# Optimization experiments

Measured on AMD Instinct MI355X. Metric: run time of the kernel, lower is better.

The kernel has to match this reference:

```python
import jax, jax.numpy as jnp
import numpy as np

B, I, H, L, D, O = 2048, 512, 512, 32, 1024, 512
TEMP = 1.0


def _make_params(key):
    ks = jax.random.split(key, 16)
    s = 0.05
    p = {}
    p['in_W'] = jax.random.normal(ks[0], (H, I), jnp.float32) * s
    p['in_b'] = jnp.zeros((H,), jnp.float32)
    p['out_W'] = jax.random.normal(ks[1], (O, H), jnp.float32) * s
    p['out_b'] = jnp.zeros((O,), jnp.float32)
    p['enc_Wih'] = jax.random.normal(ks[2], (4 * H, H), jnp.float32) * s
    p['enc_Whh'] = jax.random.normal(ks[3], (4 * H, H), jnp.float32) * s
    p['enc_bih'] = jnp.zeros((4 * H,), jnp.float32)
    p['enc_bhh'] = jnp.zeros((4 * H,), jnp.float32)
    p['dec_Wih'] = jax.random.normal(ks[4], (4 * H, H), jnp.float32) * s
    p['dec_Whh'] = jax.random.normal(ks[5], (4 * H, H), jnp.float32) * s
    p['dec_bih'] = jnp.zeros((4 * H,), jnp.float32)
    p['dec_bhh'] = jnp.zeros((4 * H,), jnp.float32)
    p['h2t_W'] = jax.random.normal(ks[6], (D, H), jnp.float32) * s
    p['h2t_b'] = jnp.zeros((D,), jnp.float32)
    p['t2h_W'] = jax.random.normal(ks[7], (H, D), jnp.float32) * s
    p['t2h_b'] = jnp.zeros((H,), jnp.float32)
    return p


def setup_inputs() -> dict:
    key = jax.random.key(0)
    k1, k2, k3 = jax.random.split(key, 3)
    inp = {'x': jax.random.normal(k1, (B, I), jnp.float32),
           'gumbel': jax.random.gumbel(k2, (L, B, D), jnp.float32)}
    inp.update(_make_params(k3))
    return inp


def _lstm_cell(x, h, c, Wih, Whh, bih, bhh):
    gates = x @ Wih.T + bih + h @ Whh.T + bhh  # [B, 4H]
    i, f, g, o = jnp.split(gates, 4, axis=-1)
    i = jax.nn.sigmoid(i); f = jax.nn.sigmoid(f)
    g = jnp.tanh(g); o = jax.nn.sigmoid(o)
    c_new = f * c + i * g
    h_new = o * jnp.tanh(c_new)
    return h_new, c_new


def reference(x, gumbel, in_W, in_b, out_W, out_b,
              enc_Wih, enc_Whh, enc_bih, enc_bhh,
              dec_Wih, dec_Whh, dec_bih, dec_bhh,
              h2t_W, h2t_b, t2h_W, t2h_b):
    # ---- encode ----
    x_emb = x @ in_W.T + in_b                      # [B, H]
    hx0 = jnp.zeros((B, H), x.dtype)
    inp0 = jnp.zeros((B, H), x.dtype)

    def enc_step(carry, g_noise):
        hx, cx, inp = carry
        hx, cx = _lstm_cell(inp, hx, cx, enc_Wih, enc_Whh, enc_bih, enc_bhh)
        pre = hx @ h2t_W.T + h2t_b                 # [B, D]
        soft = jax.nn.softmax((pre + g_noise) / TEMP, axis=-1)
        amax = jnp.argmax(soft, axis=-1)           # [B]
        oh = jax.nn.one_hot(amax, D, dtype=soft.dtype)
        z = soft + jax.lax.stop_gradient(oh - soft)  # straight-through
        inp = z @ t2h_W.T + t2h_b
        return (hx, cx, inp), (z, pre, amax)

    # initial cell state is the embedded input (cx = x), per the source
    _, (z_seq, logit_seq, msg_seq) = jax.lax.scan(
        enc_step, (hx0, x_emb, inp0), gumbel)
    one_hot = jnp.transpose(z_seq, (1, 0, 2))      # [B, L, D]
    logits = jnp.transpose(logit_seq, (1, 0, 2))   # [B, L, D]
    messages = msg_seq.T                           # [B, L]

    # ---- decode ----
    z_emb = z_seq @ t2h_W.T + t2h_b                # [L, B, H]

    def dec_step(carry, inp):
        hx, cx = carry
        hx, cx = _lstm_cell(inp, hx, cx, dec_Wih, dec_Whh, dec_bih, dec_bhh)
        return (hx, cx), None

    (hx_final, _), _ = jax.lax.scan(
        dec_step, (jnp.zeros((B, H), x.dtype), jnp.zeros((B, H), x.dtype)), z_emb)
    recon = hx_final @ out_W.T + out_b             # [B, O]
    return recon, one_hot, logits, messages
```

## Files before the change

kernel.cpp:

```cpp
#include <hip/hip_runtime.h>
#include <math.h>

#define B_  2048
#define I_  512
#define H_  512
#define L_  32
#define D_  1024
#define O_  512
#define H4_ 2048
#define KC  32

typedef _Float16 f16x8 __attribute__((ext_vector_type(8)));
typedef _Float16 f16x4 __attribute__((ext_vector_type(4)));
typedef float    f32x4 __attribute__((ext_vector_type(4)));

#define SPLIT_S  1024.0f
#define SPLIT_RS 0.0009765625f

__global__ __launch_bounds__(256) void gemm_atb(
    const float* __restrict__ A, const float* __restrict__ W,
    const float* __restrict__ bias, float* __restrict__ C, int ldc,
    float* __restrict__ C2, int ldc2,
    int M, int N, int K)
{
    __shared__ __align__(16) float As[KC][68];
    __shared__ __align__(16) float Ws[KC][68];
    const int tx = threadIdx.x & 15, ty = threadIdx.x >> 4;
    const int m0 = blockIdx.y * 64, n0 = blockIdx.x * 64;
    float acc[4][4] = {};

    for (int k0 = 0; k0 < K; k0 += KC) {
#pragma unroll
        for (int p = 0; p < 2; ++p) {
            int q = threadIdx.x + 256 * p;
            int r = q >> 3, c = q & 7;
            float4 va = *reinterpret_cast<const float4*>(
                &A[(long long)(m0 + r) * K + k0 + c * 4]);
            As[c * 4 + 0][r] = va.x; As[c * 4 + 1][r] = va.y;
            As[c * 4 + 2][r] = va.z; As[c * 4 + 3][r] = va.w;
            float4 vw = *reinterpret_cast<const float4*>(
                &W[(long long)(n0 + r) * K + k0 + c * 4]);
            Ws[c * 4 + 0][r] = vw.x; Ws[c * 4 + 1][r] = vw.y;
            Ws[c * 4 + 2][r] = vw.z; Ws[c * 4 + 3][r] = vw.w;
        }
        __syncthreads();
#pragma unroll
        for (int kk = 0; kk < KC; ++kk) {
            float4 a = *reinterpret_cast<const float4*>(&As[kk][ty * 4]);
            float4 w = *reinterpret_cast<const float4*>(&Ws[kk][tx * 4]);
            float av[4] = {a.x, a.y, a.z, a.w};
            float wv[4] = {w.x, w.y, w.z, w.w};
#pragma unroll
            for (int i = 0; i < 4; ++i)
#pragma unroll
                for (int j = 0; j < 4; ++j)
                    acc[i][j] = fmaf(av[i], wv[j], acc[i][j]);
        }
        __syncthreads();
    }

#pragma unroll
    for (int i = 0; i < 4; ++i) {
        int m = m0 + ty * 4 + i;
        int n = n0 + tx * 4;
        float4 out;
        out.x = acc[i][0]; out.y = acc[i][1]; out.z = acc[i][2]; out.w = acc[i][3];
        if (bias) {
            out.x += bias[n + 0]; out.y += bias[n + 1];
            out.z += bias[n + 2]; out.w += bias[n + 3];
        }
        *reinterpret_cast<float4*>(&C[(long long)m * ldc + n]) = out;
        if (C2)
            *reinterpret_cast<float4*>(&C2[(long long)m * ldc2 + n]) = out;
    }
}

__global__ __launch_bounds__(256) void split_f16(
    const float* __restrict__ src, _Float16* __restrict__ d1,
    _Float16* __restrict__ d2, int n4)
{
    int i = blockIdx.x * 256 + threadIdx.x;
    if (i >= n4) return;
    float4 v = reinterpret_cast<const float4*>(src)[i];
    float vv[4] = {v.x, v.y, v.z, v.w};
    f16x4 o1, o2;
#pragma unroll
    for (int j = 0; j < 4; ++j) {
        _Float16 hh = (_Float16)vv[j];
        o1[j] = hh;
        o2[j] = (_Float16)((vv[j] - (float)hh) * SPLIT_S);
    }
    *reinterpret_cast<f16x4*>(d1 + 4 * i) = o1;
    *reinterpret_cast<f16x4*>(d2 + 4 * i) = o2;
}

__global__ __launch_bounds__(512) void lstm_step_mfma(
    const _Float16* __restrict__ hx1, const _Float16* __restrict__ hx2,
    float* __restrict__ cx,
    const _Float16* __restrict__ W1, const _Float16* __restrict__ W2,
    const float* __restrict__ P,
    const int* __restrict__ m_prev,
    const float* __restrict__ bih, const float* __restrict__ bhh,
    _Float16* __restrict__ ho1, _Float16* __restrict__ ho2,
    float* __restrict__ hof)
{
    __shared__ __align__(16) _Float16 As1[128][72];
    __shared__ __align__(16) _Float16 As2[128][72];
    __shared__ __align__(16) _Float16 Ws1[128][72];
    __shared__ __align__(16) _Float16 Ws2[128][72];
    __shared__ int ms[128];

    const int tid = threadIdx.x;
    const int m0 = blockIdx.y * 128, h0 = blockIdx.x * 32;
    const int l = tid & 63, wid = tid >> 6;
    const int wm = wid >> 1, wn = wid & 1;

    if (m_prev != nullptr && tid < 128) ms[tid] = m_prev[m0 + tid];

    f32x4 accM[2][4] = {};
    f32x4 accC[2][4] = {};

    for (int k0 = 0; k0 < H_; k0 += 64) {
#pragma unroll
        for (int cc = 0; cc < 2; ++cc) {
            int c = tid + cc * 512;
            int r = c >> 3, q = (c & 7) << 3;
            size_t ga = (size_t)(m0 + r) * H_ + k0 + q;
            *(uint4*)&As1[r][q] = *(const uint4*)(hx1 + ga);
            *(uint4*)&As2[r][q] = *(const uint4*)(hx2 + ga);
            int wrow = ((r >> 4) & 3) * H_ + h0 + ((r >> 6) << 4) + (r & 15);
            size_t gw = (size_t)wrow * H_ + k0 + q;
            *(uint4*)&Ws1[r][q] = *(const uint4*)(W1 + gw);
            *(uint4*)&Ws2[r][q] = *(const uint4*)(W2 + gw);
        }
        __syncthreads();
        const int ac = (l >> 4) << 3;
        const int arow = wm * 32 + (l & 15);
        const int brow = wn * 64 + (l & 15);
#pragma unroll
        for (int kc = 0; kc < 2; ++kc) {
            int ko = kc * 32 + ac;
            f16x8 b1[4], b2[4];
#pragma unroll
            for (int fn = 0; fn < 4; ++fn) {
                b1[fn] = *(const f16x8*)&Ws1[brow + fn * 16][ko];
                b2[fn] = *(const f16x8*)&Ws2[brow + fn * 16][ko];
            }
#pragma unroll
            for (int fm = 0; fm < 2; ++fm) {
                f16x8 a1 = *(const f16x8*)&As1[arow + fm * 16][ko];
                f16x8 a2 = *(const f16x8*)&As2[arow + fm * 16][ko];
#pragma unroll
                for (int fn = 0; fn < 4; ++fn) {
                    accM[fm][fn] = __builtin_amdgcn_mfma_f32_16x16x32_f16(
                        a1, b1[fn], accM[fm][fn], 0, 0, 0);
                    accC[fm][fn] = __builtin_amdgcn_mfma_f32_16x16x32_f16(
                        a1, b2[fn], accC[fm][fn], 0, 0, 0);
                    accC[fm][fn] = __builtin_amdgcn_mfma_f32_16x16x32_f16(
                        a2, b1[fn], accC[fm][fn], 0, 0, 0);
                }
            }
        }
        __syncthreads();
    }

    const int hl = l & 15;
    const int h  = h0 + wn * 16 + hl;
    const int rb = m0 + wm * 32 + ((l >> 4) << 2);
    float bs0 = bih[0 * H_ + h] + bhh[0 * H_ + h];
    float bs1 = bih[1 * H_ + h] + bhh[1 * H_ + h];
    float bs2 = bih[2 * H_ + h] + bhh[2 * H_ + h];
    float bs3 = bih[3 * H_ + h] + bhh[3 * H_ + h];
#pragma unroll
    for (int fm = 0; fm < 2; ++fm) {
#pragma unroll
        for (int rg = 0; rg < 4; ++rg) {
            int b = rb + fm * 16 + rg;
            float g0 = accM[fm][0][rg] + SPLIT_RS * accC[fm][0][rg] + bs0;
            float g1 = accM[fm][1][rg] + SPLIT_RS * accC[fm][1][rg] + bs1;
            float g2 = accM[fm][2][rg] + SPLIT_RS * accC[fm][2][rg] + bs2;
            float g3 = accM[fm][3][rg] + SPLIT_RS * accC[fm][3][rg] + bs3;
            if (m_prev != nullptr) {
                const float* Pr = P + (size_t)ms[b - m0] * H4_;
                g0 += Pr[0 * H_ + h]; g1 += Pr[1 * H_ + h];
                g2 += Pr[2 * H_ + h]; g3 += Pr[3 * H_ + h];
            }
            float ig = 1.f / (1.f + expf(-g0));
            float fg = 1.f / (1.f + expf(-g1));
            float gg = tanhf(g2);
            float og = 1.f / (1.f + expf(-g3));
            size_t off = (size_t)b * H_ + h;
            float cnew = fg * cx[off] + ig * gg;
            cx[off] = cnew;
            float hv = og * tanhf(cnew);
            _Float16 hh1 = (_Float16)hv;
            ho1[off] = hh1;
            ho2[off] = (_Float16)((hv - (float)hh1) * SPLIT_S);
            if (hof != nullptr) hof[off] = hv;
        }
    }
}

__global__ __launch_bounds__(256) void gemm_pre_mfma(
    const _Float16* __restrict__ A1, const _Float16* __restrict__ A2,
    const _Float16* __restrict__ W1, const _Float16* __restrict__ W2,
    const float* __restrict__ bias,
    float* __restrict__ C,
    float* __restrict__ C2, int ldc2)
{
    __shared__ __align__(16) _Float16 As1[64][72];
    __shared__ __align__(16) _Float16 As2[64][72];
    __shared__ __align__(16) _Float16 Ws1[128][72];
    __shared__ __align__(16) _Float16 Ws2[128][72];

    const int tid = threadIdx.x;
    const int m0 = blockIdx.y * 64, n0 = blockIdx.x * 128;
    const int l = tid & 63, wid = tid >> 6;
    const int wm = wid >> 1, wn = wid & 1;

    f32x4 accM[2][4] = {};
    f32x4 accC[2][4] = {};

    for (int k0 = 0; k0 < H_; k0 += 64) {
#pragma unroll
        for (int cc = 0; cc < 2; ++cc) {
            int c = tid + cc * 256;
            int r = c >> 3, q = (c & 7) << 3;
            size_t ga = (size_t)(m0 + r) * H_ + k0 + q;
            *(uint4*)&As1[r][q] = *(const uint4*)(A1 + ga);
            *(uint4*)&As2[r][q] = *(const uint4*)(A2 + ga);
        }
#pragma unroll
        for (int cc = 0; cc < 4; ++cc) {
            int c = tid + cc * 256;
            int r = c >> 3, q = (c & 7) << 3;
            size_t gw = (size_t)(n0 + r) * H_ + k0 + q;
            *(uint4*)&Ws1[r][q] = *(const uint4*)(W1 + gw);
            *(uint4*)&Ws2[r][q] = *(const uint4*)(W2 + gw);
        }
        __syncthreads();
        const int ac = (l >> 4) << 3;
        const int arow = wm * 32 + (l & 15);
        const int brow = wn * 64 + (l & 15);
#pragma unroll
        for (int kc = 0; kc < 2; ++kc) {
            int ko = kc * 32 + ac;
            f16x8 b1[4], b2[4];
#pragma unroll
            for (int fn = 0; fn < 4; ++fn) {
                b1[fn] = *(const f16x8*)&Ws1[brow + fn * 16][ko];
                b2[fn] = *(const f16x8*)&Ws2[brow + fn * 16][ko];
            }
#pragma unroll
            for (int fm = 0; fm < 2; ++fm) {
                f16x8 a1 = *(const f16x8*)&As1[arow + fm * 16][ko];
                f16x8 a2 = *(const f16x8*)&As2[arow + fm * 16][ko];
#pragma unroll
                for (int fn = 0; fn < 4; ++fn) {
                    accM[fm][fn] = __builtin_amdgcn_mfma_f32_16x16x32_f16(
                        a1, b1[fn], accM[fm][fn], 0, 0, 0);
                    accC[fm][fn] = __builtin_amdgcn_mfma_f32_16x16x32_f16(
                        a1, b2[fn], accC[fm][fn], 0, 0, 0);
                    accC[fm][fn] = __builtin_amdgcn_mfma_f32_16x16x32_f16(
                        a2, b1[fn], accC[fm][fn], 0, 0, 0);
                }
            }
        }
        __syncthreads();
    }

    const int hl = l & 15;
    const int rb = m0 + wm * 32 + ((l >> 4) << 2);
#pragma unroll
    for (int fn = 0; fn < 4; ++fn) {
        int d = n0 + wn * 64 + fn * 16 + hl;
        float bv = bias[d];
#pragma unroll
        for (int fm = 0; fm < 2; ++fm)
#pragma unroll
            for (int rg = 0; rg < 4; ++rg) {
                int b = rb + fm * 16 + rg;
                float v = accM[fm][fn][rg] + SPLIT_RS * accC[fm][fn][rg] + bv;
                C[(size_t)b * D_ + d] = v;
                C2[(size_t)b * ldc2 + d] = v;
            }
    }
}

__global__ __launch_bounds__(256) void argmax_step(
    const float* __restrict__ pre, const float* __restrict__ gum,
    float* __restrict__ onehot, float* __restrict__ messages,
    int* __restrict__ m_out, int l)
{
    const int wave = threadIdx.x >> 6, lane = threadIdx.x & 63;
    const int b = blockIdx.x * 4 + wave;
    const float* pr = pre + (long long)b * D_;
    const float* gr = gum + (long long)b * D_;
    float best = -INFINITY; int bi = 0;
#pragma unroll
    for (int j = 0; j < D_ / 64; ++j) {
        int idx = lane + j * 64;
        float v = pr[idx] + gr[idx];
        if (v > best) { best = v; bi = idx; }
    }
#pragma unroll
    for (int off = 32; off > 0; off >>= 1) {
        float ov = __shfl_down(best, off);
        int   oi = __shfl_down(bi, off);
        if (ov > best || (ov == best && oi < bi)) { best = ov; bi = oi; }
    }
    if (lane == 0) {
        m_out[b] = bi;
        messages[(long long)b * L_ + l] = (float)bi;
        onehot[((long long)b * L_ + l) * D_ + bi] = 1.0f;
    }
}

__global__ __launch_bounds__(256) void build_emb(
    const float* __restrict__ t2h_W, const float* __restrict__ t2h_b,
    float* __restrict__ emb)
{
    int idx = blockIdx.x * 256 + threadIdx.x;
    int d = idx >> 9, h = idx & (H_ - 1);
    emb[idx] = t2h_W[(long long)h * D_ + d] + t2h_b[h];
}

extern "C" void kernel_launch(void* const* d_in, const int* in_sizes, int n_in,
                              void* d_out, int out_size, void* d_ws, size_t ws_size,
                              hipStream_t stream)
{
    (void)in_sizes; (void)n_in; (void)out_size; (void)ws_size;
    const float* x       = (const float*)d_in[0];
    const float* gumbel  = (const float*)d_in[1];
    const float* in_W    = (const float*)d_in[2];
    const float* in_b    = (const float*)d_in[3];
    const float* out_W   = (const float*)d_in[4];
    const float* out_b   = (const float*)d_in[5];
    const float* enc_Wih = (const float*)d_in[6];
    const float* enc_Whh = (const float*)d_in[7];
    const float* enc_bih = (const float*)d_in[8];
    const float* enc_bhh = (const float*)d_in[9];
    const float* dec_Wih = (const float*)d_in[10];
    const float* dec_Whh = (const float*)d_in[11];
    const float* dec_bih = (const float*)d_in[12];
    const float* dec_bhh = (const float*)d_in[13];
    const float* h2t_W   = (const float*)d_in[14];
    const float* h2t_b   = (const float*)d_in[15];
    const float* t2h_W   = (const float*)d_in[16];
    const float* t2h_b   = (const float*)d_in[17];

    float* out      = (float*)d_out;
    float* recon    = out;
    float* onehot   = out + (size_t)B_ * O_;
    float* logits   = onehot + (size_t)B_ * L_ * D_;
    float* messages = logits + (size_t)B_ * L_ * D_;

    float* ws    = (float*)d_ws;
    float* cx    = ws;
    float* pre   = cx + (size_t)B_ * H_;
    float* emb   = pre + (size_t)B_ * D_;
    float* P_enc = emb + (size_t)D_ * H_;
    float* P_dec = P_enc + (size_t)D_ * H4_;
    float* hxf   = P_dec + (size_t)D_ * H4_;
    int*   m_all = (int*)(hxf + (size_t)B_ * H_);
    _Float16* fb   = (_Float16*)(m_all + (size_t)L_ * B_);
    _Float16* hxA1 = fb;  fb += (size_t)B_ * H_;
    _Float16* hxA2 = fb;  fb += (size_t)B_ * H_;
    _Float16* hxB1 = fb;  fb += (size_t)B_ * H_;
    _Float16* hxB2 = fb;  fb += (size_t)B_ * H_;
    _Float16* encW1 = fb; fb += (size_t)H4_ * H_;
    _Float16* encW2 = fb; fb += (size_t)H4_ * H_;
    _Float16* decW1 = fb; fb += (size_t)H4_ * H_;
    _Float16* decW2 = fb; fb += (size_t)H4_ * H_;
    _Float16* h2t1  = fb; fb += (size_t)D_ * H_;
    _Float16* h2t2  = fb;

    const dim3 blk256(256);

    hipMemsetAsync(hxA1, 0, (size_t)B_ * H_ * 4, stream);
    hipMemsetAsync(onehot, 0, (size_t)B_ * L_ * D_ * sizeof(float), stream);

    split_f16<<<dim3((H4_ * H_ / 4) / 256), blk256, 0, stream>>>(
        enc_Whh, encW1, encW2, H4_ * H_ / 4);
    split_f16<<<dim3((H4_ * H_ / 4) / 256), blk256, 0, stream>>>(
        dec_Whh, decW1, decW2, H4_ * H_ / 4);
    split_f16<<<dim3((D_ * H_ / 4) / 256), blk256, 0, stream>>>(
        h2t_W, h2t1, h2t2, D_ * H_ / 4);

    gemm_atb<<<dim3(H_ / 64, B_ / 64), blk256, 0, stream>>>(
        x, in_W, in_b, cx, H_, nullptr, 0, B_, H_, I_);

    build_emb<<<dim3((D_ * H_) / 256), blk256, 0, stream>>>(t2h_W, t2h_b, emb);
    gemm_atb<<<dim3(H4_ / 64, D_ / 64), blk256, 0, stream>>>(
        emb, enc_Wih, nullptr, P_enc, H4_, nullptr, 0, D_, H4_, H_);
    gemm_atb<<<dim3(H4_ / 64, D_ / 64), blk256, 0, stream>>>(
        emb, dec_Wih, nullptr, P_dec, H4_, nullptr, 0, D_, H4_, H_);

    _Float16 *c1 = hxA1, *c2 = hxA2, *n1 = hxB1, *n2 = hxB2;
    for (int l = 0; l < L_; ++l) {
        lstm_step_mfma<<<dim3(H_ / 32, B_ / 128), dim3(512), 0, stream>>>(
            c1, c2, cx, encW1, encW2, P_enc,
            (l == 0) ? nullptr : (m_all + (size_t)(l - 1) * B_),
            enc_bih, enc_bhh, n1, n2, nullptr);
        { _Float16* t = c1; c1 = n1; n1 = t; t = c2; c2 = n2; n2 = t; }
        gemm_pre_mfma<<<dim3(D_ / 128, B_ / 64), blk256, 0, stream>>>(
            c1, c2, h2t1, h2t2, h2t_b, pre,
            logits + (size_t)l * D_, L_ * D_);
        argmax_step<<<dim3(B_ / 4), blk256, 0, stream>>>(
            pre, gumbel + (size_t)l * B_ * D_, onehot, messages,
            m_all + (size_t)l * B_, l);
    }

    hipMemsetAsync(c1, 0, (size_t)B_ * H_ * 2, stream);
    hipMemsetAsync(c2, 0, (size_t)B_ * H_ * 2, stream);
    hipMemsetAsync(cx, 0, (size_t)B_ * H_ * sizeof(float), stream);
    for (int l = 0; l < L_; ++l) {
        lstm_step_mfma<<<dim3(H_ / 32, B_ / 128), dim3(512), 0, stream>>>(
            c1, c2, cx, decW1, decW2, P_dec, m_all + (size_t)l * B_,
            dec_bih, dec_bhh, n1, n2, (l == L_ - 1) ? hxf : nullptr);
        { _Float16* t = c1; c1 = n1; n1 = t; t = c2; c2 = n2; n2 = t; }
    }

    gemm_atb<<<dim3(O_ / 64, B_ / 64), blk256, 0, stream>>>(
        hxf, out_W, out_b, recon, O_, nullptr, 0, B_, O_, H_);
}
```

Before: 3.209 ms.

## Fuse gumbel argmax into logits GEMM and use async global-to-LDS swizzled loads

Fuses the Gumbel-noise add and per-row partial argmax into the logits GEMM epilogue. Each column block writes a per-row best value and index, and a small kernel reduces the 8 partials. This removes the separate pass that rewrote and reread the pre buffer. Both MFMA kernels now load tiles with global_load_lds into an XOR-swizzled unpadded LDS layout, which skips the register round-trip and avoids bank conflicts. The cost is an extra gumbel read in the epilogue, a cross-lane shuffle reduction, and more intricate swizzle index math that must match between loads and fragment reads.

Result: no change. 3.169 ms (-1.2%).

```diff
diff --git a/kernel.cpp b/kernel.cpp
--- a/kernel.cpp
+++ b/kernel.cpp
@@ -16,6 +16,17 @@
 
 #define SPLIT_S  1024.0f
 #define SPLIT_RS 0.0009765625f
+
+__device__ __forceinline__ void gload16(const _Float16* g, _Float16* l) {
+    __builtin_amdgcn_global_load_lds(
+        (const __attribute__((address_space(1))) void*)g,
+        (__attribute__((address_space(3))) void*)l, 16, 0, 0);
+}
+
+__device__ __forceinline__ f16x8 lds_frag(const _Float16* base, int row, int ko) {
+    int off = row * 64 + ((((ko >> 3) ^ (row & 7))) << 3);
+    return *(const f16x8*)(base + off);
+}
 
 __global__ __launch_bounds__(256) void gemm_atb(
     const float* __restrict__ A, const float* __restrict__ W,
@@ -104,10 +115,10 @@
     _Float16* __restrict__ ho1, _Float16* __restrict__ ho2,
     float* __restrict__ hof)
 {
-    __shared__ __align__(16) _Float16 As1[128][72];
-    __shared__ __align__(16) _Float16 As2[128][72];
-    __shared__ __align__(16) _Float16 Ws1[128][72];
-    __shared__ __align__(16) _Float16 Ws2[128][72];
+    __shared__ __align__(16) _Float16 As1[128 * 64];
+    __shared__ __align__(16) _Float16 As2[128 * 64];
+    __shared__ __align__(16) _Float16 Ws1[128 * 64];
+    __shared__ __align__(16) _Float16 Ws2[128 * 64];
     __shared__ int ms[128];
 
     const int tid = threadIdx.x;
@@ -122,16 +133,17 @@
 
     for (int k0 = 0; k0 < H_; k0 += 64) {
 #pragma unroll
-        for (int cc = 0; cc < 2; ++cc) {
-            int c = tid + cc * 512;
-            int r = c >> 3, q = (c & 7) << 3;
-            size_t ga = (size_t)(m0 + r) * H_ + k0 + q;
-            *(uint4*)&As1[r][q] = *(const uint4*)(hx1 + ga);
-            *(uint4*)&As2[r][q] = *(const uint4*)(hx2 + ga);
+        for (int s = 0; s < 2; ++s) {
+            int seg = wid + s * 8;
+            int r   = seg * 8 + (l >> 3);
+            int jsw = ((l & 7) ^ (l >> 3)) << 3;
+            size_t ga = (size_t)(m0 + r) * H_ + k0 + jsw;
+            gload16(hx1 + ga, &As1[seg * 512]);
+            gload16(hx2 + ga, &As2[seg * 512]);
             int wrow = ((r >> 4) & 3) * H_ + h0 + ((r >> 6) << 4) + (r & 15);
-            size_t gw = (size_t)wrow * H_ + k0 + q;
-            *(uint4*)&Ws1[r][q] = *(const uint4*)(W1 + gw);
-            *(uint4*)&Ws2[r][q] = *(const uint4*)(W2 + gw);
+            size_t gw = (size_t)wrow * H_ + k0 + jsw;
+            gload16(W1 + gw, &Ws1[seg * 512]);
+            gload16(W2 + gw, &Ws2[seg * 512]);
         }
         __syncthreads();
         const int ac = (l >> 4) << 3;
@@ -143,13 +155,13 @@
             f16x8 b1[4], b2[4];
 #pragma unroll
             for (int fn = 0; fn < 4; ++fn) {
-                b1[fn] = *(const f16x8*)&Ws1[brow + fn * 16][ko];
-                b2[fn] = *(const f16x8*)&Ws2[brow + fn * 16][ko];
+                b1[fn] = lds_frag(Ws1, brow + fn * 16, ko);
+                b2[fn] = lds_frag(Ws2, brow + fn * 16, ko);
             }
 #pragma unroll
             for (int fm = 0; fm < 2; ++fm) {
-                f16x8 a1 = *(const f16x8*)&As1[arow + fm * 16][ko];
-                f16x8 a2 = *(const f16x8*)&As2[arow + fm * 16][ko];
+                f16x8 a1 = lds_frag(As1, arow + fm * 16, ko);
+                f16x8 a2 = lds_frag(As2, arow + fm * 16, ko);
 #pragma unroll
                 for (int fn = 0; fn < 4; ++fn) {
                     accM[fm][fn] = __builtin_amdgcn_mfma_f32_16x16x32_f16(
@@ -201,17 +213,20 @@
     }
 }
 
-__global__ __launch_bounds__(256) void gemm_pre_mfma(
+__global__ __launch_bounds__(256) void gemm_pre_fused(
     const _Float16* __restrict__ A1, const _Float16* __restrict__ A2,
     const _Float16* __restrict__ W1, const _Float16* __restrict__ W2,
     const float* __restrict__ bias,
-    float* __restrict__ C,
-    float* __restrict__ C2, int ldc2)
-{
-    __shared__ __align__(16) _Float16 As1[64][72];
-    __shared__ __align__(16) _Float16 As2[64][72];
-    __shared__ __align__(16) _Float16 Ws1[128][72];
-    __shared__ __align__(16) _Float16 Ws2[128][72];
+    float* __restrict__ C2, int ldc2,
+    const float* __restrict__ gum,
+    float* __restrict__ pbest, int* __restrict__ pidx)
+{
+    __shared__ __align__(16) _Float16 As1[64 * 64];
+    __shared__ __align__(16) _Float16 As2[64 * 64];
+    __shared__ __align__(16) _Float16 Ws1[128 * 64];
+    __shared__ __align__(16) _Float16 Ws2[128 * 64];
+    __shared__ float cb[2][64];
+    __shared__ int   ci[2][64];
 
     const int tid = threadIdx.x;
     const int m0 = blockIdx.y * 64, n0 = blockIdx.x * 128;
@@ -223,20 +238,22 @@
 
     for (int k0 = 0; k0 < H_; k0 += 64) {
 #pragma unroll
-        for (int cc = 0; cc < 2; ++cc) {
-            int c = tid + cc * 256;
-            int r = c >> 3, q = (c & 7) << 3;
-            size_t ga = (size_t)(m0 + r) * H_ + k0 + q;
-            *(uint4*)&As1[r][q] = *(const uint4*)(A1 + ga);
-            *(uint4*)&As2[r][q] = *(const uint4*)(A2 + ga);
-        }
-#pragma unroll
-        for (int cc = 0; cc < 4; ++cc) {
-            int c = tid + cc * 256;
-            int r = c >> 3, q = (c & 7) << 3;
-            size_t gw = (size_t)(n0 + r) * H_ + k0 + q;
-            *(uint4*)&Ws1[r][q] = *(const uint4*)(W1 + gw);
-            *(uint4*)&Ws2[r][q] = *(const uint4*)(W2 + gw);
+        for (int s = 0; s < 2; ++s) {
+            int seg = wid + s * 4;
+            int r   = seg * 8 + (l >> 3);
+            int jsw = ((l & 7) ^ (l >> 3)) << 3;
+            size_t ga = (size_t)(m0 + r) * H_ + k0 + jsw;
+            gload16(A1 + ga, &As1[seg * 512]);
+            gload16(A2 + ga, &As2[seg * 512]);
+        }
+#pragma unroll
+        for (int s = 0; s < 4; ++s) {
+            int seg = wid + s * 4;
+            int r   = seg * 8 + (l >> 3);
+            int jsw = ((l & 7) ^ (l >> 3)) << 3;
+            size_t gw = (size_t)(n0 + r) * H_ + k0 + jsw;
+            gload16(W1 + gw, &Ws1[seg * 512]);
+            gload16(W2 + gw, &Ws2[seg * 512]);
         }
         __syncthreads();
         const int ac = (l >> 4) << 3;
@@ -248,13 +265,13 @@
             f16x8 b1[4], b2[4];
 #pragma unroll
             for (int fn = 0; fn < 4; ++fn) {
-                b1[fn] = *(const f16x8*)&Ws1[brow + fn * 16][ko];
-                b2[fn] = *(const f16x8*)&Ws2[brow + fn * 16][ko];
+                b1[fn] = lds_frag(Ws1, brow + fn * 16, ko);
+                b2[fn] = lds_frag(Ws2, brow + fn * 16, ko);
             }
 #pragma unroll
             for (int fm = 0; fm < 2; ++fm) {
-                f16x8 a1 = *(const f16x8*)&As1[arow + fm * 16][ko];
-                f16x8 a2 = *(const f16x8*)&As2[arow + fm * 16][ko];
+                f16x8 a1 = lds_frag(As1, arow + fm * 16, ko);
+                f16x8 a2 = lds_frag(As2, arow + fm * 16, ko);
 #pragma unroll
                 for (int fn = 0; fn < 4; ++fn) {
                     accM[fm][fn] = __builtin_amdgcn_mfma_f32_16x16x32_f16(
@@ -270,7 +287,14 @@
     }
 
     const int hl = l & 15;
-    const int rb = m0 + wm * 32 + ((l >> 4) << 2);
+    const int g4 = l >> 4;
+    const int rb = m0 + wm * 32 + (g4 << 2);
+    float vbest[2][4]; int vidx[2][4];
+#pragma unroll
+    for (int fm = 0; fm < 2; ++fm)
+#pragma unroll
+        for (int rg = 0; rg < 4; ++rg) { vbest[fm][rg] = -INFINITY; vidx[fm][rg] = 0; }
+
 #pragma unroll
     for (int fn = 0; fn < 4; ++fn) {
         int d = n0 + wn * 64 + fn * 16 + hl;
@@ -281,39 +305,62 @@
             for (int rg = 0; rg < 4; ++rg) {
                 int b = rb + fm * 16 + rg;
                 float v = accM[fm][fn][rg] + SPLIT_RS * accC[fm][fn][rg] + bv;
-                C[(size_t)b * D_ + d] = v;
                 C2[(size_t)b * ldc2 + d] = v;
-            }
-    }
-}
-
-__global__ __launch_bounds__(256) void argmax_step(
-    const float* __restrict__ pre, const float* __restrict__ gum,
+                float t = v + gum[(size_t)b * D_ + d];
+                if (t > vbest[fm][rg]) { vbest[fm][rg] = t; vidx[fm][rg] = d; }
+            }
+    }
+
+#pragma unroll
+    for (int off = 1; off < 16; off <<= 1) {
+#pragma unroll
+        for (int fm = 0; fm < 2; ++fm)
+#pragma unroll
+            for (int rg = 0; rg < 4; ++rg) {
+                float ov = __shfl_xor(vbest[fm][rg], off);
+                int   oi = __shfl_xor(vidx[fm][rg], off);
+                if (ov > vbest[fm][rg] ||
+                    (ov == vbest[fm][rg] && oi < vidx[fm][rg])) {
+                    vbest[fm][rg] = ov; vidx[fm][rg] = oi;
+                }
+            }
+    }
+    if (hl == 0) {
+#pragma unroll
+        for (int fm = 0; fm < 2; ++fm)
+#pragma unroll
+            for (int rg = 0; rg < 4; ++rg) {
+                int rl = wm * 32 + fm * 16 + (g4 << 2) + rg;
+                cb[wn][rl] = vbest[fm][rg];
+                ci[wn][rl] = vidx[fm][rg];
+            }
+    }
+    __syncthreads();
+    if (tid < 64) {
+        float b0 = cb[0][tid]; int i0 = ci[0][tid];
+        float b1v = cb[1][tid]; int i1 = ci[1][tid];
+        if (b1v > b0 || (b1v == b0 && i1 < i0)) { b0 = b1v; i0 = i1; }
+        pbest[(size_t)(m0 + tid) * 8 + blockIdx.x] = b0;
+        pidx [(size_t)(m0 + tid) * 8 + blockIdx.x] = i0;
+    }
+}
+
+__global__ __launch_bounds__(256) void argmax_fin(
+    const float* __restrict__ pbest, const int* __restrict__ pidx,
     float* __restrict__ onehot, float* __restrict__ messages,
     int* __restrict__ m_out, int l)
 {
-    const int wave = threadIdx.x >> 6, lane = threadIdx.x & 63;
-    const int b = blockIdx.x * 4 + wave;
-    const float* pr = pre + (long long)b * D_;
-    const float* gr = gum + (long long)b * D_;
+    int b = blockIdx.x * 256 + threadIdx.x;
     float best = -INFINITY; int bi = 0;
 #pragma unroll
-    for (int j = 0; j < D_ / 64; ++j) {
-        int idx = lane + j * 64;
-        float v = pr[idx] + gr[idx];
-        if (v > best) { best = v; bi = idx; }
-    }
-#pragma unroll
-    for (int off = 32; off > 0; off >>= 1) {
-        float ov = __shfl_down(best, off);
-        int   oi = __shfl_down(bi, off);
-        if (ov > best || (ov == best && oi < bi)) { best = ov; bi = oi; }
-    }
-    if (lane == 0) {
-        m_out[b] = bi;
-        messages[(long long)b * L_ + l] = (float)bi;
-        onehot[((long long)b * L_ + l) * D_ + bi] = 1.0f;
-    }
+    for (int j = 0; j < 8; ++j) {
+        float v = pbest[(size_t)b * 8 + j];
+        int   i = pidx [(size_t)b * 8 + j];
+        if (v > best || (v == best && i < bi)) { best = v; bi = i; }
+    }
+    m_out[b] = bi;
+    messages[(size_t)b * L_ + l] = (float)bi;
+    onehot[((size_t)b * L_ + l) * D_ + bi] = 1.0f;
 }
 
 __global__ __launch_bounds__(256) void build_emb(
@@ -357,12 +404,13 @@
 
     float* ws    = (float*)d_ws;
     float* cx    = ws;
-    float* pre   = cx + (size_t)B_ * H_;
-    float* emb   = pre + (size_t)B_ * D_;
+    float* emb   = cx + (size_t)B_ * H_;
     float* P_enc = emb + (size_t)D_ * H_;
     float* P_dec = P_enc + (size_t)D_ * H4_;
     float* hxf   = P_dec + (size_t)D_ * H4_;
-    int*   m_all = (int*)(hxf + (size_t)B_ * H_);
+    float* pbest = hxf + (size_t)B_ * H_;
+    int*   pidx  = (int*)(pbest + (size_t)B_ * 8);
+    int*   m_all = pidx + (size_t)B_ * 8;
     _Float16* fb   = (_Float16*)(m_all + (size_t)L_ * B_);
     _Float16* hxA1 = fb;  fb += (size_t)B_ * H_;
     _Float16* hxA2 = fb;  fb += (size_t)B_ * H_;
@@ -403,12 +451,12 @@
             (l == 0) ? nullptr : (m_all + (size_t)(l - 1) * B_),
             enc_bih, enc_bhh, n1, n2, nullptr);
         { _Float16* t = c1; c1 = n1; n1 = t; t = c2; c2 = n2; n2 = t; }
-        gemm_pre_mfma<<<dim3(D_ / 128, B_ / 64), blk256, 0, stream>>>(
-            c1, c2, h2t1, h2t2, h2t_b, pre,
-            logits + (size_t)l * D_, L_ * D_);
-        argmax_step<<<dim3(B_ / 4), blk256, 0, stream>>>(
-            pre, gumbel + (size_t)l * B_ * D_, onehot, messages,
-            m_all + (size_t)l * B_, l);
+        gemm_pre_fused<<<dim3(D_ / 128, B_ / 64), blk256, 0, stream>>>(
+            c1, c2, h2t1, h2t2, h2t_b,
+            logits + (size_t)l * D_, L_ * D_,
+            gumbel + (size_t)l * B_ * D_, pbest, pidx);
+        argmax_fin<<<dim3(B_ / 256), blk256, 0, stream>>>(
+            pbest, pidx, onehot, messages, m_all + (size_t)l * B_, l);
     }
 
     hipMemsetAsync(c1, 0, (size_t)B_ * H_ * 2, stream);
```
